# Optimization experiments

Measured on AMD Instinct MI355X. Metric: run time of the kernel, lower is better.

Reference implementation:

```python
import jax, jax.numpy as jnp
import numpy as np

IMG = 640
C = 80
K = 10
LB, LC = 7.5, 0.5
ALPHA_COST, BETA_COST = 0.5, 6.0
GAMMA, ALPHA = 2.0, 0.25
EPS = 1e-7
PI = 3.141592653589793


def xywh_to_xyxy(b):
    cx, cy, w, h = b[..., 0], b[..., 1], b[..., 2], b[..., 3]
    return jnp.stack([cx - w * 0.5, cy - h * 0.5, cx + w * 0.5, cy + h * 0.5], axis=-1)


def bbox_iou(box1, box2):
    # box1 [M,4], box2 [N,4] xyxy -> [M,N]
    area1 = jnp.clip(box1[:, 2] - box1[:, 0], 0) * jnp.clip(box1[:, 3] - box1[:, 1], 0)
    area2 = jnp.clip(box2[:, 2] - box2[:, 0], 0) * jnp.clip(box2[:, 3] - box2[:, 1], 0)
    ix1 = jnp.maximum(box1[:, None, 0], box2[None, :, 0])
    iy1 = jnp.maximum(box1[:, None, 1], box2[None, :, 1])
    ix2 = jnp.minimum(box1[:, None, 2], box2[None, :, 2])
    iy2 = jnp.minimum(box1[:, None, 3], box2[None, :, 3])
    inter = jnp.clip(ix2 - ix1, 0) * jnp.clip(iy2 - iy1, 0)
    union = area1[:, None] + area2[None, :] - inter + EPS
    return jnp.clip(inter / union, 0.0, 1.0)


def bbox_ciou(p, t):
    # elementwise [N,4] x [N,4] xyxy -> [N]
    px1, py1, px2, py2 = p[:, 0], p[:, 1], p[:, 2], p[:, 3]
    tx1, ty1, tx2, ty2 = t[:, 0], t[:, 1], t[:, 2], t[:, 3]
    pw = jnp.clip(px2 - px1, EPS)
    ph = jnp.clip(py2 - py1, EPS)
    tw = jnp.clip(tx2 - tx1, EPS)
    th = jnp.clip(ty2 - ty1, EPS)
    inter = jnp.clip(jnp.minimum(px2, tx2) - jnp.maximum(px1, tx1), 0) * \
            jnp.clip(jnp.minimum(py2, ty2) - jnp.maximum(py1, ty1), 0)
    union = pw * ph + tw * th - inter + EPS
    iou = inter / union
    cd = ((px1 + px2) * 0.5 - (tx1 + tx2) * 0.5) ** 2 + ((py1 + py2) * 0.5 - (ty1 + ty2) * 0.5) ** 2
    cw = jnp.maximum(px2, tx2) - jnp.minimum(px1, tx1)
    ch = jnp.maximum(py2, ty2) - jnp.minimum(py1, ty1)
    c2 = cw ** 2 + ch ** 2 + EPS
    v = (4.0 / PI ** 2) * (jnp.arctan(tw / th) - jnp.arctan(pw / ph)) ** 2
    alpha = jax.lax.stop_gradient(v / (v - iou + 1.0 + EPS))
    return iou - cd / c2 - alpha * v


def _decode(p, stride):
    # p: [B, A, S, S, E] -> box [B, A*S*S, 4] (xywh px), cls [B, A*S*S, C]
    B, A, S, _, E = p.shape
    tx, ty, tw, th = p[..., 0], p[..., 1], p[..., 2], p[..., 3]
    gy, gx = jnp.meshgrid(jnp.arange(S, dtype=p.dtype), jnp.arange(S, dtype=p.dtype), indexing='ij')
    gx = gx.reshape(1, 1, S, S)
    gy = gy.reshape(1, 1, S, S)
    px = (jax.nn.sigmoid(tx) * 2.0 - 0.5 + gx) * stride  # center_mode='v8'
    py = (jax.nn.sigmoid(ty) * 2.0 - 0.5 + gy) * stride
    pw = jax.nn.softplus(tw) * stride                      # wh_mode='softplus'
    ph = jax.nn.softplus(th) * stride
    box = jnp.stack([px, py, pw, ph], axis=-1).reshape(B, -1, 4)
    cls = p[..., 4:].reshape(B, -1, C)
    return box, cls


def _per_image(p_box, p_logits, gt, labels):
    # p_box [M,4] xywh, p_logits [M,C], gt [N,4] xyxy, labels [N]
    N = gt.shape[0]
    tcx = (gt[:, 0] + gt[:, 2]) * 0.5
    tcy = (gt[:, 1] + gt[:, 3]) * 0.5
    dist = (p_box[:, 0][:, None] - tcx[None, :]) ** 2 + (p_box[:, 1][:, None] - tcy[None, :]) ** 2  # [M,N]
    _, cand = jax.lax.top_k(-dist.T, K)       # [N,K] nearest anchors per target
    cand = cand.reshape(-1)                    # [N*K] (dups don't change the min)
    cand_box = p_box[cand]
    cand_logits = p_logits[cand]
    cls_score = jax.nn.sigmoid(cand_logits)[:, labels]          # [NK,N]
    iou = bbox_iou(xywh_to_xyxy(cand_box), gt)                  # [NK,N]
    cost = ALPHA_COST * (1.0 - cls_score) + BETA_COST * (1.0 - iou)
    matched = cand[jnp.argmin(cost, axis=0)]                    # [N]
    ciou = bbox_ciou(xywh_to_xyxy(p_box[matched]), gt)
    loss_box = LB * jnp.sum(1.0 - ciou) / N
    tgt = jnp.zeros_like(p_logits).at[matched, labels].set(1.0)  # [M,C]
    x = p_logits
    ce = jnp.maximum(x, 0) - x * tgt + jnp.log1p(jnp.exp(-jnp.abs(x)))
    pr = jax.nn.sigmoid(x)
    p_t = pr * tgt + (1 - pr) * (1 - tgt)
    fl = ce * (1 - p_t) ** GAMMA
    a_t = ALPHA * tgt + (1 - ALPHA) * (1 - tgt)
    loss_cls = LC * jnp.sum(a_t * fl) / N
    return loss_box + loss_cls


def _forward(p0, p1, p2, gt_boxes, labels):
    boxes, logits = [], []
    for p in (p0, p1, p2):
        S = p.shape[2]
        pb, pl = _decode(p, float(IMG) / S)
        boxes.append(pb)
        logits.append(pl)
    flat_boxes = jnp.concatenate(boxes, axis=1)    # [B, 8400, 4]
    flat_logits = jnp.concatenate(logits, axis=1)  # [B, 8400, C]
    per_img = jax.vmap(_per_image)(flat_boxes, flat_logits, gt_boxes, labels)  # [B]
    return jnp.mean(per_img)


def setup_inputs() -> dict:
    key = jax.random.key(0)
    k0, k1, k2, kc, kw, kl = jax.random.split(key, 6)
    B, N = 16, 60
    p0 = jax.random.normal(k0, (B, 1, 80, 80, 84), dtype=jnp.float32)
    p1 = jax.random.normal(k1, (B, 1, 40, 40, 84), dtype=jnp.float32)
    p2 = jax.random.normal(k2, (B, 1, 20, 20, 84), dtype=jnp.float32)
    c = jax.random.uniform(kc, (B, N, 2), minval=64.0, maxval=576.0)
    wh = jax.random.uniform(kw, (B, N, 2), minval=8.0, maxval=128.0)
    gt_boxes = jnp.concatenate([c - wh * 0.5, c + wh * 0.5], axis=-1).astype(jnp.float32)
    labels = jax.random.randint(kl, (B, N), 0, 80, dtype=jnp.int32)
    return {"p0": p0, "p1": p1, "p2": p2, "gt_boxes": gt_boxes, "labels": labels}


def reference(p0, p1, p2, gt_boxes, labels):
    return _forward(p0, p1, p2, gt_boxes, labels)
```

## Files before the change

### kernel.cpp

```cpp
#include <hip/hip_runtime.h>
#include <cfloat>
#include <math.h>

#define NB   16
#define NGT  60
#define NA   8400
#define KNN  10
#define NCAND (NGT*KNN)
#define EPSF 1e-7f
#define PIF  3.14159265358979f
#define MATCH_BLOCKS 960
#define FOCAL_BLOCKS 2100
#define TOPK_BLOCKS  240

#define NV0   2150400u
#define NV1    537600u
#define NV2    134400u
#define FOCAL_COUNT 2688000u

#define LOG2E 1.44269504088896341f
#define LN2   0.69314718055994531f

__device__ __forceinline__ float fexp2(float x){ return __builtin_amdgcn_exp2f(x); }
__device__ __forceinline__ float flog2(float x){ return __builtin_amdgcn_logf(x); }
__device__ __forceinline__ float frcp (float x){ return __builtin_amdgcn_rcpf(x); }

__device__ __forceinline__ float fsigm(float x){
  return frcp(1.0f + fexp2(-x*LOG2E));
}
__device__ __forceinline__ float fsoftplus(float x){
  float u = fexp2(-fabsf(x)*LOG2E);
  return fmaxf(x,0.f) + LN2*flog2(1.0f + u);
}
__device__ __forceinline__ float fbg(float x){
  float u = fexp2(fminf(-x*LOG2E, 126.0f));
  float t = frcp(1.0f + u);
  return (x + LN2*flog2(1.0f + u)) * t * t;
}

__device__ __forceinline__ float focal_fbg4(const float* __restrict__ p0,
                                            const float* __restrict__ p1,
                                            const float* __restrict__ p2, unsigned u){
  unsigned g = u / 20u;
  unsigned v = 21u*g + (u - 20u*g) + 1u;
  const float* p; unsigned vloc;
  if (v < NV0)          { p=p0; vloc = v; }
  else if (v < NV0+NV1) { p=p1; vloc = v - NV0; }
  else                  { p=p2; vloc = v - (NV0+NV1); }
  float4 x4 = *(const float4*)(p + (size_t)vloc*4u);
  return fbg(x4.x) + fbg(x4.y) + fbg(x4.z) + fbg(x4.w);
}

struct ARow { const float* q; float stf; int i, j; };
__device__ __forceinline__ ARow anchor_row(const float* p0,const float* p1,const float* p2,int img,int a){
  ARow r;
  if (a < 6400){ int l=a;      r.q = p0 + (size_t)(img*6400 + l)*84; r.stf= 8.f; r.i=l/80; r.j=l-80*r.i; }
  else if (a < 8000){ int l=a-6400; r.q = p1 + (size_t)(img*1600 + l)*84; r.stf=16.f; r.i=l/40; r.j=l-40*r.i; }
  else { int l=a-8000;         r.q = p2 + (size_t)(img*400  + l)*84; r.stf=32.f; r.i=l/20; r.j=l-20*r.i; }
  return r;
}
__device__ __forceinline__ float4 decode_box_xywh(const ARow& r){
  float4 x4 = *(const float4*)r.q;
  float px = (fsigm(x4.x)*2.f - 0.5f + (float)r.j)*r.stf;
  float py = (fsigm(x4.y)*2.f - 0.5f + (float)r.i)*r.stf;
  float pw = fsoftplus(x4.z)*r.stf;
  float ph = fsoftplus(x4.w)*r.stf;
  return make_float4(px,py,pw,ph);
}

__global__ __launch_bounds__(256) void topk_kernel(const float* __restrict__ p0,
                                                   const float* __restrict__ p1,
                                                   const float* __restrict__ p2,
                                                   const float* __restrict__ gt,
                                                   int* __restrict__ cand){
  int wid  = threadIdx.x >> 6;
  int lane = threadIdx.x & 63;
  int pair = blockIdx.x*4 + wid;
  int img = pair / NGT, g = pair - img*NGT;
  const float* gb = gt + (size_t)(img*NGT + g)*4;
  float tcx = (gb[0]+gb[2])*0.5f, tcy = (gb[1]+gb[3])*0.5f;

  int jx0 = (int)(tcx * 0.125f),   iy0 = (int)(tcy * 0.125f);
  int jx1 = (int)(tcx * 0.0625f),  iy1 = (int)(tcy * 0.0625f);
  int jx2 = (int)(tcx * 0.03125f), iy2 = (int)(tcy * 0.03125f);

  float d0=FLT_MAX,d1=FLT_MAX,d2=FLT_MAX,d3=FLT_MAX;
  int   a0,a1,a2,a3;
  #pragma unroll
  for (int s=0; s<4; s++){
    int c = lane + 64*s;
    float dd = FLT_MAX; int aa = 9000000 + c;
    const float* p; int i, j, S, base, rowmul, valid = 1; float stf;
    if (c < 169)      { int r=c/13,  q=c-13*r;           i=iy0-6+r; j=jx0-6+q; S=80; base=0;    p=p0; rowmul=6400; stf= 8.f; }
    else if (c < 218) { int t=c-169; int r=t/7, q=t-7*r; i=iy1-3+r; j=jx1-3+q; S=40; base=6400; p=p1; rowmul=1600; stf=16.f; }
    else if (c < 243) { int t=c-218; int r=t/5, q=t-5*r; i=iy2-2+r; j=jx2-2+q; S=20; base=8000; p=p2; rowmul=400;  stf=32.f; }
    else { valid = 0; i=j=0; S=1; base=0; p=p0; rowmul=0; stf=0.f; }
    if (valid && i>=0 && i<S && j>=0 && j<S){
      int local = i*S + j;
      const float* q4 = p + (size_t)(img*rowmul + local)*84u;
      float2 xy = *(const float2*)q4;
      float px = (fsigm(xy.x)*2.f - 0.5f + (float)j)*stf;
      float py = (fsigm(xy.y)*2.f - 0.5f + (float)i)*stf;
      float dx=px-tcx, dy=py-tcy;
      dd = dx*dx + dy*dy;
      aa = base + local;
    }
    if (s==0){ d0=dd; a0=aa; } else if (s==1){ d1=dd; a1=aa; }
    else if (s==2){ d2=dd; a2=aa; } else { d3=dd; a3=aa; }
  }

  for (int r=0; r<KNN; r++){
    float v = d0; int anc = a0;
    if (d1 < v || (d1==v && a1<anc)){ v=d1; anc=a1; }
    if (d2 < v || (d2==v && a2<anc)){ v=d2; anc=a2; }
    if (d3 < v || (d3==v && a3<anc)){ v=d3; anc=a3; }
    #pragma unroll
    for (int off=32; off>0; off>>=1){
      float v2 = __shfl_xor(v, off);
      int  A2 = __shfl_xor(anc, off);
      if (v2 < v || (v2==v && A2<anc)){ v=v2; anc=A2; }
    }
    if (a0==anc) d0=FLT_MAX;
    if (a1==anc) d1=FLT_MAX;
    if (a2==anc) d2=FLT_MAX;
    if (a3==anc) d3=FLT_MAX;
    if (lane == 0) cand[(size_t)pair*KNN + r] = anc;
  }
}

__global__ __launch_bounds__(256) void focal_match_kernel(const float* __restrict__ p0,
                                                          const float* __restrict__ p1,
                                                          const float* __restrict__ p2,
                                                          const float* __restrict__ gt,
                                                          const int* __restrict__ labels,
                                                          const int* __restrict__ cand,
                                                          int* __restrict__ matched,
                                                          float* __restrict__ fsum){
  if (blockIdx.x < FOCAL_BLOCKS){
    __shared__ float sbuf[4];
    const unsigned S = FOCAL_BLOCKS*256u;
    unsigned u = blockIdx.x*256u + threadIdx.x;
    float s0 = focal_fbg4(p0,p1,p2, u);
    float s1 = focal_fbg4(p0,p1,p2, u +   S);
    float s2 = focal_fbg4(p0,p1,p2, u + 2*S);
    float s3 = focal_fbg4(p0,p1,p2, u + 3*S);
    float s4 = focal_fbg4(p0,p1,p2, u + 4*S);
    float sum = ((s0 + s1) + (s2 + s3)) + s4;
    sum *= 0.75f;
    #pragma unroll
    for (int off=32; off>0; off>>=1) sum += __shfl_xor(sum, off);
    int wid = threadIdx.x >> 6;
    if ((threadIdx.x & 63) == 0) sbuf[wid] = sum;
    __syncthreads();
    if (threadIdx.x == 0) fsum[blockIdx.x] = sbuf[0]+sbuf[1]+sbuf[2]+sbuf[3];
    return;
  }

  int bid2 = blockIdx.x - FOCAL_BLOCKS;
  int img = bid2 & 15;
  int j   = bid2 >> 4;
  int tid = threadIdx.x;
  int wid = tid >> 6, lane = tid & 63;
  const float* gb = gt + (size_t)(img*NGT + j)*4;
  float gx=gb[0], gy=gb[1], gz=gb[2], gw=gb[3];
  float a2 = fmaxf(gz-gx,0.f)*fmaxf(gw-gy,0.f);
  int lab = labels[img*NGT + j];

  const int* ci = cand + (size_t)img*NCAND;
  float best = FLT_MAX; int bslot = 1<<30; int banchor = -1;
  for (int c=tid; c<NCAND; c+=256){
    int a = ci[c];
    ARow ar = anchor_row(p0,p1,p2,img,a);
    float4 b = decode_box_xywh(ar);
    float bx1=b.x-b.z*0.5f, by1=b.y-b.w*0.5f, bx2=b.x+b.z*0.5f, by2=b.y+b.w*0.5f;
    float a1 = fmaxf(bx2-bx1,0.f)*fmaxf(by2-by1,0.f);
    float ix1=fmaxf(bx1,gx), iy1=fmaxf(by1,gy);
    float ix2=fminf(bx2,gz), iy2=fminf(by2,gw);
    float inter = fmaxf(ix2-ix1,0.f)*fmaxf(iy2-iy1,0.f);
    float uni = a1 + a2 - inter + EPSF;
    float iou = fminf(fmaxf(inter/uni,0.f),1.f);
    float lg = ar.q[4+lab];
    float cost = 0.5f*(1.f - fsigm(lg)) + 6.f*(1.f - iou);
    if (cost < best){ best=cost; bslot=c; banchor=a; }
  }
  #pragma unroll
  for (int off=32; off>0; off>>=1){
    float v2 = __shfl_xor(best, off);
    int  s2 = __shfl_xor(bslot, off);
    int  a2s= __shfl_xor(banchor, off);
    if (v2 < best || (v2==best && s2<bslot)){ best=v2; bslot=s2; banchor=a2s; }
  }
  __shared__ float bc[4]; __shared__ int bs[4], ba[4];
  if (lane == 0){ bc[wid]=best; bs[wid]=bslot; ba[wid]=banchor; }
  __syncthreads();
  if (tid == 0){
    float v=bc[0]; int s=bs[0]; int a=ba[0];
    #pragma unroll
    for (int k=1;k<4;k++){
      if (bc[k] < v || (bc[k]==v && bs[k]<s)){ v=bc[k]; s=bs[k]; a=ba[k]; }
    }
    matched[img*NGT + j] = a;
  }
}

__global__ __launch_bounds__(1024) void tail_kernel(const int* __restrict__ matched_g,
                                                    const float* __restrict__ gt,
                                                    const int* __restrict__ labels,
                                                    const float* __restrict__ p0,
                                                    const float* __restrict__ p1,
                                                    const float* __restrict__ p2,
                                                    const float* __restrict__ fsum,
                                                    float* __restrict__ out){
  int tid = threadIdx.x;
  int wid = tid >> 6;
  int lane = tid & 63;
  __shared__ int sm[NB][NGT];
  __shared__ int sl[NB][NGT];
  __shared__ float wb[NB], wc[NB], wf[NB];
  if (lane < NGT){
    sm[wid][lane] = matched_g[wid*NGT + lane];
    sl[wid][lane] = labels[wid*NGT + lane];
  }
  __syncthreads();

  int img = wid;
  float local_box = 0.f, local_corr = 0.f;
  if (lane < NGT){
    int j = lane;
    int m = sm[img][j];
    ARow ar = anchor_row(p0,p1,p2,img,m);
    float4 pb = decode_box_xywh(ar);
    float px1=pb.x-pb.z*0.5f, py1=pb.y-pb.w*0.5f, px2=pb.x+pb.z*0.5f, py2=pb.y+pb.w*0.5f;
    const float* gb = gt + (size_t)(img*NGT + j)*4;
    float gx=gb[0], gy=gb[1], gz=gb[2], gw=gb[3];
    float pw=fmaxf(px2-px1,EPSF), ph=fmaxf(py2-py1,EPSF);
    float tw=fmaxf(gz-gx,EPSF),  th=fmaxf(gw-gy,EPSF);
    float inter = fmaxf(fminf(px2,gz)-fmaxf(px1,gx),0.f)*fmaxf(fminf(py2,gw)-fmaxf(py1,gy),0.f);
    float uni = pw*ph + tw*th - inter + EPSF;
    float iou = inter/uni;
    float dcx = (px1+px2)*0.5f - (gx+gz)*0.5f;
    float dcy = (py1+py2)*0.5f - (gy+gw)*0.5f;
    float cd = dcx*dcx + dcy*dcy;
    float cw = fmaxf(px2,gz) - fminf(px1,gx);
    float ch = fmaxf(py2,gw) - fminf(py1,gy);
    float c2 = cw*cw + ch*ch + EPSF;
    float dv = atanf(tw/th) - atanf(pw/ph);
    float v  = (4.f/(PIF*PIF))*dv*dv;
    float alpha = v/(v - iou + 1.f + EPSF);
    float ciou = iou - cd/c2 - alpha*v;
    local_box = 1.f - ciou;

    int lab = sl[img][j];
    bool dup = false;
    for (int j2=0; j2<j; j2++)
      if (sm[img][j2]==m && sl[img][j2]==lab){ dup=true; break; }
    if (!dup){
      float x = ar.q[4+lab];
      float s  = fsigm(x);
      float u  = fexp2(-fabsf(x)*LOG2E);
      float lt = LN2*flog2(1.0f + u);
      float sp_pos = fmaxf(-x,0.f) + lt;
      float sp_neg = fmaxf( x,0.f) + lt;
      local_corr = 0.25f*sp_pos*(1.f-s)*(1.f-s) - 0.75f*sp_neg*s*s;
    }
  }
  float local_f = fsum[tid] + fsum[tid + 1024];
  if (tid < FOCAL_BLOCKS - 2048) local_f += fsum[tid + 2048];
  #pragma unroll
  for (int off=32; off>0; off>>=1){
    local_box  += __shfl_xor(local_box,  off);
    local_corr += __shfl_xor(local_corr, off);
    local_f    += __shfl_xor(local_f,    off);
  }
  if (lane == 0){ wb[wid]=local_box; wc[wid]=local_corr; wf[wid]=local_f; }
  __syncthreads();
  if (tid == 0){
    float sb=0.f, sc=0.f, sf=0.f;
    #pragma unroll
    for (int k=0;k<NB;k++){ sb+=wb[k]; sc+=wc[k]; sf+=wf[k]; }
    out[0] = (7.5f*sb + 0.5f*(sf + sc)) / (60.f*16.f);
  }
}

extern "C" void kernel_launch(void* const* d_in, const int* in_sizes, int n_in,
                              void* d_out, int out_size, void* d_ws, size_t ws_size,
                              hipStream_t stream){
  const float* p0 = (const float*)d_in[0];
  const float* p1 = (const float*)d_in[1];
  const float* p2 = (const float*)d_in[2];
  const float* gt = (const float*)d_in[3];
  const int* labels = (const int*)d_in[4];
  float* out = (float*)d_out;

  int*   cand    = (int*)d_ws;
  int*   matched = (int*)((char*)cand + (size_t)NB*NCAND*sizeof(int));
  float* fsum    = (float*)((char*)matched + (size_t)NB*NGT*sizeof(int));

  topk_kernel<<<TOPK_BLOCKS, 256, 0, stream>>>(p0, p1, p2, gt, cand);
  focal_match_kernel<<<FOCAL_BLOCKS + MATCH_BLOCKS, 256, 0, stream>>>(p0, p1, p2, gt, labels,
                                                                      cand, matched, fsum);
  tail_kernel<<<1, 1024, 0, stream>>>(matched, gt, labels, p0, p1, p2, fsum, out);
}
```

Before: 43.48 us.

## Merge topk and matching into focal kernel, reduce match partials in tail

```diff
diff --git a/kernel.cpp b/kernel.cpp
--- a/kernel.cpp
+++ b/kernel.cpp
@@ -9,9 +9,10 @@
 #define NCAND (NGT*KNN)
 #define EPSF 1e-7f
 #define PIF  3.14159265358979f
-#define MATCH_BLOCKS 960
-#define FOCAL_BLOCKS 2100
-#define TOPK_BLOCKS  240
+
+#define FOCAL_BLOCKS  2100
+#define SPARSE_BLOCKS 240
+#define K1_BLOCKS (FOCAL_BLOCKS + SPARSE_BLOCKS)
 
 #define NV0   2150400u
 #define NV1    537600u
@@ -68,14 +69,36 @@
   return make_float4(px,py,pw,ph);
 }
 
-__global__ __launch_bounds__(256) void topk_kernel(const float* __restrict__ p0,
-                                                   const float* __restrict__ p1,
-                                                   const float* __restrict__ p2,
-                                                   const float* __restrict__ gt,
-                                                   int* __restrict__ cand){
+__global__ __launch_bounds__(256) void k1_kernel(const float* __restrict__ p0,
+                                                 const float* __restrict__ p1,
+                                                 const float* __restrict__ p2,
+                                                 const float* __restrict__ gt,
+                                                 const int* __restrict__ labels,
+                                                 int* __restrict__ cand,
+                                                 unsigned long long* __restrict__ partials,
+                                                 float* __restrict__ fsum){
+  if (blockIdx.x < FOCAL_BLOCKS){
+    __shared__ float sbuf[4];
+    const unsigned S = FOCAL_BLOCKS*256u;
+    unsigned u = blockIdx.x*256u + threadIdx.x;
+    float s0 = focal_fbg4(p0,p1,p2, u);
+    float s1 = focal_fbg4(p0,p1,p2, u +   S);
+    float s2 = focal_fbg4(p0,p1,p2, u + 2*S);
+    float s3 = focal_fbg4(p0,p1,p2, u + 3*S);
+    float s4 = focal_fbg4(p0,p1,p2, u + 4*S);
+    float sum = (((s0 + s1) + (s2 + s3)) + s4) * 0.75f;
+    #pragma unroll
+    for (int off=32; off>0; off>>=1) sum += __shfl_xor(sum, off);
+    int wid = threadIdx.x >> 6;
+    if ((threadIdx.x & 63) == 0) sbuf[wid] = sum;
+    __syncthreads();
+    if (threadIdx.x == 0) fsum[blockIdx.x] = sbuf[0]+sbuf[1]+sbuf[2]+sbuf[3];
+    return;
+  }
+
   int wid  = threadIdx.x >> 6;
   int lane = threadIdx.x & 63;
-  int pair = blockIdx.x*4 + wid;
+  int pair = (blockIdx.x - FOCAL_BLOCKS)*4 + wid;
   int img = pair / NGT, g = pair - img*NGT;
   const float* gb = gt + (size_t)(img*NGT + g)*4;
   float tcx = (gb[0]+gb[2])*0.5f, tcy = (gb[1]+gb[3])*0.5f;
@@ -109,6 +132,8 @@
     else if (s==2){ d2=dd; a2=aa; } else { d3=dd; a3=aa; }
   }
 
+  int anc_r[KNN];
+  #pragma unroll
   for (int r=0; r<KNN; r++){
     float v = d0; int anc = a0;
     if (d1 < v || (d1==v && a1<anc)){ v=d1; anc=a1; }
@@ -124,106 +149,69 @@
     if (a1==anc) d1=FLT_MAX;
     if (a2==anc) d2=FLT_MAX;
     if (a3==anc) d3=FLT_MAX;
+    anc_r[r] = anc;
     if (lane == 0) cand[(size_t)pair*KNN + r] = anc;
   }
-}
-
-__global__ __launch_bounds__(256) void focal_match_kernel(const float* __restrict__ p0,
-                                                          const float* __restrict__ p1,
-                                                          const float* __restrict__ p2,
-                                                          const float* __restrict__ gt,
-                                                          const int* __restrict__ labels,
-                                                          const int* __restrict__ cand,
-                                                          int* __restrict__ matched,
-                                                          float* __restrict__ fsum){
-  if (blockIdx.x < FOCAL_BLOCKS){
-    __shared__ float sbuf[4];
-    const unsigned S = FOCAL_BLOCKS*256u;
-    unsigned u = blockIdx.x*256u + threadIdx.x;
-    float s0 = focal_fbg4(p0,p1,p2, u);
-    float s1 = focal_fbg4(p0,p1,p2, u +   S);
-    float s2 = focal_fbg4(p0,p1,p2, u + 2*S);
-    float s3 = focal_fbg4(p0,p1,p2, u + 3*S);
-    float s4 = focal_fbg4(p0,p1,p2, u + 4*S);
-    float sum = ((s0 + s1) + (s2 + s3)) + s4;
-    sum *= 0.75f;
-    #pragma unroll
-    for (int off=32; off>0; off>>=1) sum += __shfl_xor(sum, off);
-    int wid = threadIdx.x >> 6;
-    if ((threadIdx.x & 63) == 0) sbuf[wid] = sum;
-    __syncthreads();
-    if (threadIdx.x == 0) fsum[blockIdx.x] = sbuf[0]+sbuf[1]+sbuf[2]+sbuf[3];
-    return;
-  }
-
-  int bid2 = blockIdx.x - FOCAL_BLOCKS;
-  int img = bid2 & 15;
-  int j   = bid2 >> 4;
-  int tid = threadIdx.x;
-  int wid = tid >> 6, lane = tid & 63;
-  const float* gb = gt + (size_t)(img*NGT + j)*4;
-  float gx=gb[0], gy=gb[1], gz=gb[2], gw=gb[3];
-  float a2 = fmaxf(gz-gx,0.f)*fmaxf(gw-gy,0.f);
-  int lab = labels[img*NGT + j];
-
-  const int* ci = cand + (size_t)img*NCAND;
-  float best = FLT_MAX; int bslot = 1<<30; int banchor = -1;
-  for (int c=tid; c<NCAND; c+=256){
-    int a = ci[c];
+
+  bool jv = (lane < NGT);
+  float4 gbj = make_float4(0.f,0.f,0.f,0.f);
+  int labj = 0;
+  if (jv){
+    gbj  = *(const float4*)(gt + (size_t)(img*NGT + lane)*4);
+    labj = labels[img*NGT + lane];
+  }
+  float a2g = fmaxf(gbj.z-gbj.x,0.f)*fmaxf(gbj.w-gbj.y,0.f);
+  unsigned long long best = ~0ull;
+  #pragma unroll
+  for (int r=0; r<KNN; r++){
+    int a = anc_r[r];
     ARow ar = anchor_row(p0,p1,p2,img,a);
     float4 b = decode_box_xywh(ar);
     float bx1=b.x-b.z*0.5f, by1=b.y-b.w*0.5f, bx2=b.x+b.z*0.5f, by2=b.y+b.w*0.5f;
     float a1 = fmaxf(bx2-bx1,0.f)*fmaxf(by2-by1,0.f);
-    float ix1=fmaxf(bx1,gx), iy1=fmaxf(by1,gy);
-    float ix2=fminf(bx2,gz), iy2=fminf(by2,gw);
+    float ix1=fmaxf(bx1,gbj.x), iy1=fmaxf(by1,gbj.y);
+    float ix2=fminf(bx2,gbj.z), iy2=fminf(by2,gbj.w);
     float inter = fmaxf(ix2-ix1,0.f)*fmaxf(iy2-iy1,0.f);
-    float uni = a1 + a2 - inter + EPSF;
+    float uni = a1 + a2g - inter + EPSF;
     float iou = fminf(fmaxf(inter/uni,0.f),1.f);
-    float lg = ar.q[4+lab];
+    float lg = ar.q[4+labj];
     float cost = 0.5f*(1.f - fsigm(lg)) + 6.f*(1.f - iou);
-    if (cost < best){ best=cost; bslot=c; banchor=a; }
-  }
-  #pragma unroll
-  for (int off=32; off>0; off>>=1){
-    float v2 = __shfl_xor(best, off);
-    int  s2 = __shfl_xor(bslot, off);
-    int  a2s= __shfl_xor(banchor, off);
-    if (v2 < best || (v2==best && s2<bslot)){ best=v2; bslot=s2; banchor=a2s; }
-  }
-  __shared__ float bc[4]; __shared__ int bs[4], ba[4];
-  if (lane == 0){ bc[wid]=best; bs[wid]=bslot; ba[wid]=banchor; }
-  __syncthreads();
-  if (tid == 0){
-    float v=bc[0]; int s=bs[0]; int a=ba[0];
-    #pragma unroll
-    for (int k=1;k<4;k++){
-      if (bc[k] < v || (bc[k]==v && bs[k]<s)){ v=bc[k]; s=bs[k]; a=ba[k]; }
-    }
-    matched[img*NGT + j] = a;
-  }
-}
-
-__global__ __launch_bounds__(1024) void tail_kernel(const int* __restrict__ matched_g,
-                                                    const float* __restrict__ gt,
-                                                    const int* __restrict__ labels,
-                                                    const float* __restrict__ p0,
-                                                    const float* __restrict__ p1,
-                                                    const float* __restrict__ p2,
-                                                    const float* __restrict__ fsum,
-                                                    float* __restrict__ out){
+    unsigned long long pk = ((unsigned long long)__float_as_uint(cost) << 32)
+                          | (unsigned)(g*KNN + r);
+    if (pk < best) best = pk;
+  }
+  if (jv) partials[((size_t)img*NGT + g)*NGT + lane] = best;
+}
+
+__global__ __launch_bounds__(1024) void k2_kernel(const unsigned long long* __restrict__ partials,
+                                                  const int* __restrict__ cand,
+                                                  const float* __restrict__ gt,
+                                                  const int* __restrict__ labels,
+                                                  const float* __restrict__ p0,
+                                                  const float* __restrict__ p1,
+                                                  const float* __restrict__ p2,
+                                                  const float* __restrict__ fsum,
+                                                  float* __restrict__ out){
   int tid = threadIdx.x;
   int wid = tid >> 6;
   int lane = tid & 63;
   __shared__ int sm[NB][NGT];
   __shared__ int sl[NB][NGT];
   __shared__ float wb[NB], wc[NB], wf[NB];
+  int img = wid;
   if (lane < NGT){
-    sm[wid][lane] = matched_g[wid*NGT + lane];
-    sl[wid][lane] = labels[wid*NGT + lane];
+    unsigned long long best = ~0ull;
+    #pragma unroll 4
+    for (int g2=0; g2<NGT; g2++){
+      unsigned long long v = partials[((size_t)img*NGT + g2)*NGT + lane];
+      if (v < best) best = v;
+    }
+    int slot = (int)(best & 0xffffffffull);
+    sm[img][lane] = cand[img*NCAND + slot];
+    sl[img][lane] = labels[img*NGT + lane];
   }
   __syncthreads();
 
-  int img = wid;
   float local_box = 0.f, local_corr = 0.f;
   if (lane < NGT){
     int j = lane;
@@ -292,12 +280,10 @@
   const int* labels = (const int*)d_in[4];
   float* out = (float*)d_out;
 
-  int*   cand    = (int*)d_ws;
-  int*   matched = (int*)((char*)cand + (size_t)NB*NCAND*sizeof(int));
-  float* fsum    = (float*)((char*)matched + (size_t)NB*NGT*sizeof(int));
-
-  topk_kernel<<<TOPK_BLOCKS, 256, 0, stream>>>(p0, p1, p2, gt, cand);
-  focal_match_kernel<<<FOCAL_BLOCKS + MATCH_BLOCKS, 256, 0, stream>>>(p0, p1, p2, gt, labels,
-                                                                      cand, matched, fsum);
-  tail_kernel<<<1, 1024, 0, stream>>>(matched, gt, labels, p0, p1, p2, fsum, out);
-}
+  unsigned long long* partials = (unsigned long long*)d_ws;
+  float* fsum = (float*)((char*)d_ws + (size_t)NB*NGT*NGT*8);
+  int*   cand = (int*)((char*)fsum + FOCAL_BLOCKS*sizeof(float));
+
+  k1_kernel<<<K1_BLOCKS, 256, 0, stream>>>(p0, p1, p2, gt, labels, cand, partials, fsum);
+  k2_kernel<<<1, 1024, 0, stream>>>(partials, cand, gt, labels, p0, p1, p2, fsum, out);
+}
```

New measurement: 47.54 us. 9.3% more time.
